# Kernel optimization log

Measured on AMD Instinct MI355X. Metric: run time of the kernel, lower is better.

Reference implementation:

```python
import jax, jax.numpy as jnp
import numpy as np

B, T, IN, OUT, R = 8, 2048, 4096, 4096, 64


def setup_inputs() -> dict:
    key = jax.random.key(0)
    ks = jax.random.split(key, 6)
    x = jax.random.normal(ks[0], (B, T, IN), dtype=jnp.float32)
    weight_main = jax.random.normal(ks[1], (OUT, IN), dtype=jnp.float32) * (1.0 / np.sqrt(IN))
    U = jax.random.normal(ks[2], (OUT, R), dtype=jnp.float32) * 0.02
    S = jax.random.uniform(ks[3], (R,), dtype=jnp.float32)
    V = jax.random.normal(ks[4], (R, IN), dtype=jnp.float32) * 0.02
    bias = jax.random.normal(ks[5], (OUT,), dtype=jnp.float32) * 0.01
    return {"x": x, "weight_main": weight_main, "U": U, "S": S, "V": V, "bias": bias}


def reference(x, weight_main, U, S, V, bias):
    # residual_weight = einsum('ij,j,jk->ik', U, S, V): full [out, in] materialization
    residual_weight = jnp.einsum('ij,j,jk->ik', U, S, V)
    weight = weight_main + residual_weight
    # F.linear: x @ weight.T + bias
    return jnp.einsum('bti,oi->bto', x, weight) + bias
```

## Files before the change

kernel.cpp:

```cpp
#include <hip/hip_runtime.h>
#include <hip/hip_bf16.h>
#include <stdint.h>

#define DI __device__ __forceinline__

typedef __attribute__((ext_vector_type(4))) float f32x4;
typedef __attribute__((ext_vector_type(8))) short bf16x8;
typedef __attribute__((ext_vector_type(4))) short s16x4;

typedef unsigned short ushort_t;

constexpr int M_ = 16384;
constexpr int N_ = 4096;
constexpr int K_ = 4096;
constexpr int R_ = 64;

constexpr int BM = 256, BN = 256, BK = 64;
constexpr int NSEG = 3;
constexpr int NT_SEG = K_ / BK;
constexpr int TOT_T = NSEG * NT_SEG;

DI ushort_t f32_to_bf16_rne(float f) {
    unsigned u = __builtin_bit_cast(unsigned, f);
    u += 0x7FFFu + ((u >> 16) & 1u);
    return (ushort_t)(u >> 16);
}
DI float bf16_to_f32(ushort_t h) {
    return __builtin_bit_cast(float, (unsigned)h << 16);
}

DI void async_cp16(const void* g, void* l) {
    __builtin_amdgcn_global_load_lds(
        (const __attribute__((address_space(1))) unsigned*)g,
        (__attribute__((address_space(3))) unsigned*)l, 16, 0, 0);
}

#define BAR() do { asm volatile("" ::: "memory"); \
                   __builtin_amdgcn_s_barrier(); \
                   asm volatile("" ::: "memory"); } while (0)
#define MID() do { BAR(); \
                   asm volatile("s_waitcnt lgkmcnt(0)" ::: "memory"); \
                   __builtin_amdgcn_sched_barrier(0); \
                   __builtin_amdgcn_s_setprio(1); } while (0)
#define ENDP() do { __builtin_amdgcn_s_setprio(0); BAR(); } while (0)

__global__ __launch_bounds__(256) void k_fold_us(const float* __restrict__ U,
                                                 const float* __restrict__ S,
                                                 float* __restrict__ US) {
    int i = blockIdx.x * 256 + threadIdx.x;
    if (i < N_ * R_) US[i] = U[i] * S[i & (R_ - 1)];
}

__global__ __launch_bounds__(256) void k_fuse_w(const float* __restrict__ WM,
                                                const float* __restrict__ US,
                                                const float* __restrict__ V,
                                                ushort_t* __restrict__ hiW,
                                                ushort_t* __restrict__ loW) {
    __shared__ __align__(16) float sUS[64][68];
    __shared__ __align__(16) float sV[64][128];
    int t = threadIdx.x;
    int n0 = (blockIdx.x >> 5) * 64;
    int k0 = (blockIdx.x & 31) * 128;
#pragma unroll
    for (int j = 0; j < 4; ++j) {
        int f = j * 1024 + t * 4;
        int r = f >> 6, c = f & 63;
        *(f32x4*)&sUS[r][c] = *(const f32x4*)&US[(size_t)(n0 + r) * R_ + c];
    }
#pragma unroll
    for (int j = 0; j < 8; ++j) {
        int f = j * 1024 + t * 4;
        int r = f >> 7, c = f & 127;
        *(f32x4*)&sV[r][c] = *(const f32x4*)&V[(size_t)r * K_ + k0 + c];
    }
    __syncthreads();
    int tn = t >> 5;
    int tk = t & 31;
    float acc[8][4] = {};
    for (int r = 0; r < R_; ++r) {
        f32x4 vv = *(const f32x4*)&sV[r][tk * 4];
#pragma unroll
        for (int a = 0; a < 8; ++a) {
            float u = sUS[tn * 8 + a][r];
#pragma unroll
            for (int c = 0; c < 4; ++c) acc[a][c] += u * vv[c];
        }
    }
#pragma unroll
    for (int a = 0; a < 8; ++a) {
        int n = n0 + tn * 8 + a;
        int k = k0 + tk * 4;
        f32x4 wmv = *(const f32x4*)&WM[(size_t)n * K_ + k];
        s16x4 h4, l4;
#pragma unroll
        for (int c = 0; c < 4; ++c) {
            float w = wmv[c] + acc[a][c];
            ushort_t h = f32_to_bf16_rne(w);
            h4[c] = (short)h;
            l4[c] = (short)f32_to_bf16_rne(w - bf16_to_f32(h));
        }
        *(s16x4*)&hiW[(size_t)n * K_ + k] = h4;
        *(s16x4*)&loW[(size_t)n * K_ + k] = l4;
    }
}

__global__ __launch_bounds__(256) void k_split_x(const float* __restrict__ X,
                                                 ushort_t* __restrict__ hiA,
                                                 ushort_t* __restrict__ loA) {
    size_t i = ((size_t)blockIdx.x * 256 + threadIdx.x) * 8;
    f32x4 a = *(const f32x4*)&X[i];
    f32x4 b = *(const f32x4*)&X[i + 4];
    bf16x8 h, l;
#pragma unroll
    for (int j = 0; j < 4; ++j) {
        ushort_t ha = f32_to_bf16_rne(a[j]);
        ushort_t hb = f32_to_bf16_rne(b[j]);
        h[j]     = (short)ha;
        h[4 + j] = (short)hb;
        l[j]     = (short)f32_to_bf16_rne(a[j] - bf16_to_f32(ha));
        l[4 + j] = (short)f32_to_bf16_rne(b[j] - bf16_to_f32(hb));
    }
    *(bf16x8*)&hiA[i] = h;
    *(bf16x8*)&loA[i] = l;
}

__global__ __launch_bounds__(512, 2) void k_gemm_8ph(const ushort_t* __restrict__ hiA,
                                                     const ushort_t* __restrict__ loA,
                                                     const ushort_t* __restrict__ hiW,
                                                     const ushort_t* __restrict__ loW,
                                                     const float* __restrict__ bias,
                                                     float* __restrict__ out) {
    __shared__ __align__(16) ushort_t lA[2][BM * BK];
    __shared__ __align__(16) ushort_t lB[2][BN * BK];

    int bid = blockIdx.x;
    int wg  = (bid & 7) * (gridDim.x >> 3) + (bid >> 3);
    int m0  = (wg >> 4) * BM;
    int n0  = (wg & 15) * BN;

    int tid  = threadIdx.x;
    int lane = tid & 63;
    int w    = tid >> 6;
    int wr   = w >> 2;
    int wc   = w & 3;
    int fr   = lane & 15;
    int fq   = lane >> 4;

    f32x4 acc[8][4] = {};

    auto stageA = [&](int tau, int h) {
        int seg = tau >> 6;
        const ushort_t* As = (seg == 1) ? loA : hiA;
        int k0 = (tau & (NT_SEG - 1)) * BK;
        ushort_t* dst = &lA[tau & 1][h * (128 * 64)];
#pragma unroll
        for (int j = 0; j < 2; ++j) {
            int ci  = j * 512 + tid;
            int row = ci >> 3, pc = ci & 7;
            int lc  = pc ^ (row & 7);
            async_cp16(&As[(size_t)(m0 + h * 128 + row) * K_ + k0 + lc * 8], &dst[ci * 8]);
        }
    };
    auto stageB = [&](int tau, int h) {
        int seg = tau >> 6;
        const ushort_t* Bs = (seg == 2) ? loW : hiW;
        int k0 = (tau & (NT_SEG - 1)) * BK;
        ushort_t* dst = &lB[tau & 1][h * (128 * 64)];
#pragma unroll
        for (int j = 0; j < 2; ++j) {
            int ci  = j * 512 + tid;
            int row = ci >> 3, pc = ci & 7;
            int lc  = pc ^ (row & 7);
            async_cp16(&Bs[(size_t)(n0 + h * 128 + row) * K_ + k0 + lc * 8], &dst[ci * 8]);
        }
    };
    auto rdA = [&](const ushort_t* la, int i, int ks) -> bf16x8 {
        int row = wr * 128 + i * 16 + fr;
        return *(const bf16x8*)&la[row * 64 + (((ks * 4 + fq) ^ (row & 7)) << 3)];
    };
    auto rdB = [&](const ushort_t* lb, int j, int ks) -> bf16x8 {
        int row = wc * 64 + j * 16 + fr;
        return *(const bf16x8*)&lb[row * 64 + (((ks * 4 + fq) ^ (row & 7)) << 3)];
    };

    bf16x8 aF[4][2];
    bf16x8 bE[2][2];
    bf16x8 bO[2][2];

    stageB(0, 0); stageB(0, 1); stageA(0, 0); stageA(0, 1);
    stageB(1, 0); stageB(1, 1);
    asm volatile("s_waitcnt vmcnt(4)" ::: "memory");
    BAR();

    const ushort_t* la0 = lA[0]; const ushort_t* lb0 = lB[0];
    const ushort_t* la1 = lA[1]; const ushort_t* lb1 = lB[1];

    constexpr int NIT = TOT_T / 2;
    for (int it = 0; it < NIT; ++it) {
        int to = 2 * it + 1;
        int ne = (2 * it + 2) % TOT_T;
        int no = (2 * it + 3) % TOT_T;

#pragma unroll
        for (int i = 0; i < 4; ++i) { aF[i][0] = rdA(la0, i, 0); aF[i][1] = rdA(la0, i, 1); }
#pragma unroll
        for (int j = 0; j < 2; ++j) { bE[j][0] = rdB(lb0, j, 0); bE[j][1] = rdB(lb0, j, 1); }
        stageA(to, 0);
        asm volatile("s_waitcnt lgkmcnt(8)" ::: "memory");
        MID();
#pragma unroll
        for (int i = 0; i < 4; ++i)
#pragma unroll
            for (int j = 0; j < 2; ++j)
#pragma unroll
                for (int ks = 0; ks < 2; ++ks)
                    acc[i][j] = __builtin_amdgcn_mfma_f32_16x16x32_bf16(aF[i][ks], bE[j][ks], acc[i][j], 0, 0, 0);
        ENDP();

#pragma unroll
        for (int j = 0; j < 2; ++j) { bO[j][0] = rdB(lb0, 2 + j, 0); bO[j][1] = rdB(lb0, 2 + j, 1); }
        stageA(to, 1);
        MID();
#pragma unroll
        for (int i = 0; i < 4; ++i)
#pragma unroll
            for (int j = 0; j < 2; ++j)
#pragma unroll
                for (int ks = 0; ks < 2; ++ks)
                    acc[i][2 + j] = __builtin_amdgcn_mfma_f32_16x16x32_bf16(aF[i][ks], bO[j][ks], acc[i][2 + j], 0, 0, 0);
        ENDP();

#pragma unroll
        for (int i = 0; i < 4; ++i) { aF[i][0] = rdA(la0, 4 + i, 0); aF[i][1] = rdA(la0, 4 + i, 1); }
        stageB(ne, 0);
        MID();
#pragma unroll
        for (int i = 0; i < 4; ++i)
#pragma unroll
            for (int j = 0; j < 2; ++j)
#pragma unroll
                for (int ks = 0; ks < 2; ++ks)
                    acc[4 + i][2 + j] = __builtin_amdgcn_mfma_f32_16x16x32_bf16(aF[i][ks], bO[j][ks], acc[4 + i][2 + j], 0, 0, 0);
        ENDP();

        stageB(ne, 1);
        asm volatile("s_waitcnt vmcnt(4)" ::: "memory");
        MID();
#pragma unroll
        for (int i = 0; i < 4; ++i)
#pragma unroll
            for (int j = 0; j < 2; ++j)
#pragma unroll
                for (int ks = 0; ks < 2; ++ks)
                    acc[4 + i][j] = __builtin_amdgcn_mfma_f32_16x16x32_bf16(aF[i][ks], bE[j][ks], acc[4 + i][j], 0, 0, 0);
        ENDP();

#pragma unroll
        for (int i = 0; i < 4; ++i) { aF[i][0] = rdA(la1, i, 0); aF[i][1] = rdA(la1, i, 1); }
#pragma unroll
        for (int j = 0; j < 2; ++j) { bE[j][0] = rdB(lb1, j, 0); bE[j][1] = rdB(lb1, j, 1); }
        stageA(ne, 0);
        asm volatile("s_waitcnt lgkmcnt(8)" ::: "memory");
        MID();
#pragma unroll
        for (int i = 0; i < 4; ++i)
#pragma unroll
            for (int j = 0; j < 2; ++j)
#pragma unroll
                for (int ks = 0; ks < 2; ++ks)
                    acc[i][j] = __builtin_amdgcn_mfma_f32_16x16x32_bf16(aF[i][ks], bE[j][ks], acc[i][j], 0, 0, 0);
        ENDP();

#pragma unroll
        for (int j = 0; j < 2; ++j) { bO[j][0] = rdB(lb1, 2 + j, 0); bO[j][1] = rdB(lb1, 2 + j, 1); }
        stageA(ne, 1);
        MID();
#pragma unroll
        for (int i = 0; i < 4; ++i)
#pragma unroll
            for (int j = 0; j < 2; ++j)
#pragma unroll
                for (int ks = 0; ks < 2; ++ks)
                    acc[i][2 + j] = __builtin_amdgcn_mfma_f32_16x16x32_bf16(aF[i][ks], bO[j][ks], acc[i][2 + j], 0, 0, 0);
        ENDP();

#pragma unroll
        for (int i = 0; i < 4; ++i) { aF[i][0] = rdA(la1, 4 + i, 0); aF[i][1] = rdA(la1, 4 + i, 1); }
        stageB(no, 0);
        MID();
#pragma unroll
        for (int i = 0; i < 4; ++i)
#pragma unroll
            for (int j = 0; j < 2; ++j)
#pragma unroll
                for (int ks = 0; ks < 2; ++ks)
                    acc[4 + i][2 + j] = __builtin_amdgcn_mfma_f32_16x16x32_bf16(aF[i][ks], bO[j][ks], acc[4 + i][2 + j], 0, 0, 0);
        ENDP();

        stageB(no, 1);
        asm volatile("s_waitcnt vmcnt(4)" ::: "memory");
        MID();
#pragma unroll
        for (int i = 0; i < 4; ++i)
#pragma unroll
            for (int j = 0; j < 2; ++j)
#pragma unroll
                for (int ks = 0; ks < 2; ++ks)
                    acc[4 + i][j] = __builtin_amdgcn_mfma_f32_16x16x32_bf16(aF[i][ks], bE[j][ks], acc[4 + i][j], 0, 0, 0);
        ENDP();
    }

    asm volatile("s_waitcnt vmcnt(0)" ::: "memory");

    float bcol[4];
#pragma unroll
    for (int j = 0; j < 4; ++j) bcol[j] = bias[n0 + wc * 64 + j * 16 + fr];
#pragma unroll
    for (int i = 0; i < 8; ++i) {
        int gm = m0 + wr * 128 + i * 16 + fq * 4;
#pragma unroll
        for (int j = 0; j < 4; ++j) {
            int gn = n0 + wc * 64 + j * 16 + fr;
#pragma unroll
            for (int r2 = 0; r2 < 4; ++r2)
                out[(size_t)(gm + r2) * N_ + gn] = acc[i][j][r2] + bcol[j];
        }
    }
}

__global__ __launch_bounds__(256, 2) void k_gemm_small(const float* __restrict__ X,
                                                       const ushort_t* __restrict__ hiW,
                                                       const ushort_t* __restrict__ loW,
                                                       const float* __restrict__ bias,
                                                       float* __restrict__ out) {
    __shared__ __align__(16) ushort_t lA[128 * 64];
    __shared__ __align__(16) ushort_t lB[128 * 64];
    int bid = blockIdx.x;
    int cpx = gridDim.x >> 3;
    int wg  = (bid & 7) * cpx + (bid >> 3);
    constexpr int NBN = N_ / 128;
    int m0 = (wg / NBN) * 128;
    int n0 = (wg % NBN) * 128;
    int tid  = threadIdx.x;
    int lane = tid & 63;
    int w    = tid >> 6;
    int wr   = w >> 1, wc = w & 1;
    int fr   = lane & 15;
    int fq   = lane >> 4;
    f32x4 acc[4][4] = {};
    for (int seg = 0; seg < 3; ++seg) {
        const ushort_t* Bs = (seg == 2) ? loW : hiW;
        bool wantLo = (seg == 1);
        for (int kt = 0; kt < K_ / 64; ++kt) {
            int k0 = kt * 64;
#pragma unroll
            for (int j = 0; j < 4; ++j) {
                int f = j * 2048 + tid * 8;
                int row = f >> 6, col = f & 63;
                async_cp16(&Bs[(size_t)(n0 + row) * K_ + k0 + col], &lB[f]);
            }
#pragma unroll
            for (int j = 0; j < 4; ++j) {
                int f = j * 2048 + tid * 8;
                int row = f >> 6, c = f & 63;
                const float* xp = &X[(size_t)(m0 + row) * K_ + k0 + c];
                f32x4 x0 = *(const f32x4*)xp;
                f32x4 x1 = *(const f32x4*)(xp + 4);
                bf16x8 o;
#pragma unroll
                for (int e = 0; e < 4; ++e) {
                    ushort_t h0 = f32_to_bf16_rne(x0[e]);
                    ushort_t h1 = f32_to_bf16_rne(x1[e]);
                    o[e]     = (short)(wantLo ? f32_to_bf16_rne(x0[e] - bf16_to_f32(h0)) : h0);
                    o[4 + e] = (short)(wantLo ? f32_to_bf16_rne(x1[e] - bf16_to_f32(h1)) : h1);
                }
                *(bf16x8*)&lA[f] = o;
            }
            __syncthreads();
#pragma unroll
            for (int ks = 0; ks < 2; ++ks) {
                bf16x8 af[4], bfv[4];
#pragma unroll
                for (int i = 0; i < 4; ++i) {
                    af[i]  = *(const bf16x8*)&lA[(wr * 64 + i * 16 + fr) * 64 + ks * 32 + fq * 8];
                    bfv[i] = *(const bf16x8*)&lB[(wc * 64 + i * 16 + fr) * 64 + ks * 32 + fq * 8];
                }
#pragma unroll
                for (int i = 0; i < 4; ++i)
#pragma unroll
                    for (int j = 0; j < 4; ++j)
                        acc[i][j] = __builtin_amdgcn_mfma_f32_16x16x32_bf16(af[i], bfv[j], acc[i][j], 0, 0, 0);
            }
            __syncthreads();
        }
    }
    float bcol[4];
#pragma unroll
    for (int j = 0; j < 4; ++j) bcol[j] = bias[n0 + wc * 64 + j * 16 + fr];
#pragma unroll
    for (int i = 0; i < 4; ++i) {
        int gm = m0 + wr * 64 + i * 16 + fq * 4;
#pragma unroll
        for (int j = 0; j < 4; ++j) {
            int gn = n0 + wc * 64 + j * 16 + fr;
#pragma unroll
            for (int r2 = 0; r2 < 4; ++r2)
                out[(size_t)(gm + r2) * N_ + gn] = acc[i][j][r2] + bcol[j];
        }
    }
}

__global__ __launch_bounds__(256) void k_naive(const float* __restrict__ X,
                                               const float* __restrict__ WM,
                                               const float* __restrict__ U,
                                               const float* __restrict__ S,
                                               const float* __restrict__ V,
                                               const float* __restrict__ bias,
                                               float* __restrict__ out) {
    __shared__ __align__(16) float sX[64][68];
    __shared__ __align__(16) float sW[64][68];
    __shared__ __align__(16) float sV[64][68];
    int t = threadIdx.x;
    int m0 = (blockIdx.x >> 6) * 64;
    int n0 = (blockIdx.x & 63) * 64;
    int tm = t >> 4, tn = t & 15;
    float acc[4][4] = {}, pacc[4][4] = {};
    for (int kc = 0; kc < K_ / 64; ++kc) {
        __syncthreads();
#pragma unroll
        for (int j = 0; j < 4; ++j) {
            int f = j * 1024 + t * 4;
            int r = f >> 6, c = f & 63;
            *(f32x4*)&sX[r][c] = *(const f32x4*)&X[(size_t)(m0 + r) * K_ + kc * 64 + c];
            *(f32x4*)&sW[r][c] = *(const f32x4*)&WM[(size_t)(n0 + r) * K_ + kc * 64 + c];
            *(f32x4*)&sV[r][c] = *(const f32x4*)&V[(size_t)r * K_ + kc * 64 + c];
        }
        __syncthreads();
        for (int k4 = 0; k4 < 16; ++k4) {
            f32x4 xa[4], wb[4], vb[4];
#pragma unroll
            for (int a = 0; a < 4; ++a) xa[a] = *(const f32x4*)&sX[tm * 4 + a][k4 * 4];
#pragma unroll
            for (int b = 0; b < 4; ++b) {
                wb[b] = *(const f32x4*)&sW[tn * 4 + b][k4 * 4];
                vb[b] = *(const f32x4*)&sV[tn * 4 + b][k4 * 4];
            }
#pragma unroll
            for (int a = 0; a < 4; ++a)
#pragma unroll
                for (int b = 0; b < 4; ++b)
#pragma unroll
                    for (int e = 0; e < 4; ++e) {
                        acc[a][b]  += xa[a][e] * wb[b][e];
                        pacc[a][b] += xa[a][e] * vb[b][e];
                    }
        }
    }
    __syncthreads();
#pragma unroll
    for (int j = 0; j < 4; ++j) {
        int f = j * 1024 + t * 4;
        int nl = f >> 6, r = f & 63;
        f32x4 uu = *(const f32x4*)&U[(size_t)(n0 + nl) * R_ + r];
        f32x4 ss = *(const f32x4*)&S[r];
        f32x4 us = uu * ss;
        *(f32x4*)&sV[nl][r] = us;
    }
#pragma unroll
    for (int a = 0; a < 4; ++a)
#pragma unroll
        for (int b = 0; b < 4; ++b) sW[tm * 4 + a][tn * 4 + b] = pacc[a][b];
    __syncthreads();
#pragma unroll
    for (int a = 0; a < 4; ++a)
#pragma unroll
        for (int b = 0; b < 4; ++b) {
            float s2 = acc[a][b];
            for (int r = 0; r < R_; ++r) s2 += sW[tm * 4 + a][r] * sV[tn * 4 + b][r];
            out[(size_t)(m0 + tm * 4 + a) * N_ + n0 + tn * 4 + b] = s2 + bias[n0 + tn * 4 + b];
        }
}

extern "C" void kernel_launch(void* const* d_in, const int* in_sizes, int n_in,
                              void* d_out, int out_size, void* d_ws, size_t ws_size,
                              hipStream_t stream) {
    const float* x    = (const float*)d_in[0];
    const float* wm   = (const float*)d_in[1];
    const float* U    = (const float*)d_in[2];
    const float* S    = (const float*)d_in[3];
    const float* V    = (const float*)d_in[4];
    const float* bias = (const float*)d_in[5];
    float* out = (float*)d_out;

    const size_t szA  = (size_t)M_ * K_ * 2;
    const size_t szW  = (size_t)N_ * K_ * 2;
    const size_t szUS = (size_t)N_ * R_ * 4;

    if (ws_size >= 2 * szA + 2 * szW + szUS) {
        ushort_t* hiA = (ushort_t*)d_ws;
        ushort_t* loA = (ushort_t*)((char*)d_ws + szA);
        ushort_t* hiW = (ushort_t*)((char*)d_ws + 2 * szA);
        ushort_t* loW = (ushort_t*)((char*)d_ws + 2 * szA + szW);
        float*    US  = (float*)((char*)d_ws + 2 * szA + 2 * szW);
        k_fold_us<<<dim3((N_ * R_ + 255) / 256), dim3(256), 0, stream>>>(U, S, US);
        k_fuse_w<<<dim3((N_ / 64) * (K_ / 128)), dim3(256), 0, stream>>>(wm, US, V, hiW, loW);
        k_split_x<<<dim3(M_ * K_ / 2048), dim3(256), 0, stream>>>(x, hiA, loA);
        k_gemm_8ph<<<dim3((M_ / BM) * (N_ / BN)), dim3(512), 0, stream>>>(
            hiA, loA, hiW, loW, bias, out);
    } else if (ws_size >= 2 * szW + szUS) {
        ushort_t* hiW = (ushort_t*)d_ws;
        ushort_t* loW = (ushort_t*)((char*)d_ws + szW);
        float*    US  = (float*)((char*)d_ws + 2 * szW);
        k_fold_us<<<dim3((N_ * R_ + 255) / 256), dim3(256), 0, stream>>>(U, S, US);
        k_fuse_w<<<dim3((N_ / 64) * (K_ / 128)), dim3(256), 0, stream>>>(wm, US, V, hiW, loW);
        k_gemm_small<<<dim3((M_ / 128) * (N_ / 128)), dim3(256), 0, stream>>>(
            x, hiW, loW, bias, out);
    } else {
        k_naive<<<dim3((M_ / 64) * (N_ / 64)), dim3(256), 0, stream>>>(x, wm, U, S, V, bias, out);
    }
}
```

Baseline: 1.873 ms.

## Prefetch LDS fragments one phase ahead in GEMM loop and fold U*S into fuse kernel

```diff
diff --git a/kernel.cpp b/kernel.cpp
--- a/kernel.cpp
+++ b/kernel.cpp
@@ -44,15 +44,9 @@
                    __builtin_amdgcn_s_setprio(1); } while (0)
 #define ENDP() do { __builtin_amdgcn_s_setprio(0); BAR(); } while (0)
 
-__global__ __launch_bounds__(256) void k_fold_us(const float* __restrict__ U,
-                                                 const float* __restrict__ S,
-                                                 float* __restrict__ US) {
-    int i = blockIdx.x * 256 + threadIdx.x;
-    if (i < N_ * R_) US[i] = U[i] * S[i & (R_ - 1)];
-}
-
 __global__ __launch_bounds__(256) void k_fuse_w(const float* __restrict__ WM,
-                                                const float* __restrict__ US,
+                                                const float* __restrict__ U,
+                                                const float* __restrict__ S,
                                                 const float* __restrict__ V,
                                                 ushort_t* __restrict__ hiW,
                                                 ushort_t* __restrict__ loW) {
@@ -65,7 +59,9 @@
     for (int j = 0; j < 4; ++j) {
         int f = j * 1024 + t * 4;
         int r = f >> 6, c = f & 63;
-        *(f32x4*)&sUS[r][c] = *(const f32x4*)&US[(size_t)(n0 + r) * R_ + c];
+        f32x4 uu = *(const f32x4*)&U[(size_t)(n0 + r) * R_ + c];
+        f32x4 ss = *(const f32x4*)&S[c];
+        *(f32x4*)&sUS[r][c] = uu * ss;
     }
 #pragma unroll
     for (int j = 0; j < 8; ++j) {
@@ -183,17 +179,30 @@
         return *(const bf16x8*)&lb[row * 64 + (((ks * 4 + fq) ^ (row & 7)) << 3)];
     };
 
-    bf16x8 aF[4][2];
-    bf16x8 bE[2][2];
-    bf16x8 bO[2][2];
+    bf16x8 aX[4], aY[4], bX[4], bY[4];
+
+#define RD_A(dst, la, ib, ks) do { \
+    dst[0] = rdA(la, (ib) + 0, ks); dst[1] = rdA(la, (ib) + 1, ks); \
+    dst[2] = rdA(la, (ib) + 2, ks); dst[3] = rdA(la, (ib) + 3, ks); } while (0)
+#define RD_B(dst, lb, ks) do { \
+    dst[0] = rdB(lb, 0, ks); dst[1] = rdB(lb, 1, ks); \
+    dst[2] = rdB(lb, 2, ks); dst[3] = rdB(lb, 3, ks); } while (0)
+#define MFMA16(IB, A_, B_) do { \
+    _Pragma("unroll") \
+    for (int i_ = 0; i_ < 4; ++i_) \
+        _Pragma("unroll") \
+        for (int j_ = 0; j_ < 4; ++j_) \
+            acc[(IB) + i_][j_] = __builtin_amdgcn_mfma_f32_16x16x32_bf16( \
+                A_[i_], B_[j_], acc[(IB) + i_][j_], 0, 0, 0); } while (0)
+
+    const ushort_t* la0 = lA[0]; const ushort_t* lb0 = lB[0];
+    const ushort_t* la1 = lA[1]; const ushort_t* lb1 = lB[1];
 
     stageB(0, 0); stageB(0, 1); stageA(0, 0); stageA(0, 1);
     stageB(1, 0); stageB(1, 1);
     asm volatile("s_waitcnt vmcnt(4)" ::: "memory");
     BAR();
-
-    const ushort_t* la0 = lA[0]; const ushort_t* lb0 = lB[0];
-    const ushort_t* la1 = lA[1]; const ushort_t* lb1 = lB[1];
+    RD_A(aX, la0, 0, 0); RD_B(bX, lb0, 0);
 
     constexpr int NIT = TOT_T / 2;
     for (int it = 0; it < NIT; ++it) {
@@ -201,116 +210,55 @@
         int ne = (2 * it + 2) % TOT_T;
         int no = (2 * it + 3) % TOT_T;
 
-#pragma unroll
-        for (int i = 0; i < 4; ++i) { aF[i][0] = rdA(la0, i, 0); aF[i][1] = rdA(la0, i, 1); }
-#pragma unroll
-        for (int j = 0; j < 2; ++j) { bE[j][0] = rdB(lb0, j, 0); bE[j][1] = rdB(lb0, j, 1); }
         stageA(to, 0);
-        asm volatile("s_waitcnt lgkmcnt(8)" ::: "memory");
-        MID();
-#pragma unroll
-        for (int i = 0; i < 4; ++i)
-#pragma unroll
-            for (int j = 0; j < 2; ++j)
-#pragma unroll
-                for (int ks = 0; ks < 2; ++ks)
-                    acc[i][j] = __builtin_amdgcn_mfma_f32_16x16x32_bf16(aF[i][ks], bE[j][ks], acc[i][j], 0, 0, 0);
-        ENDP();
-
-#pragma unroll
-        for (int j = 0; j < 2; ++j) { bO[j][0] = rdB(lb0, 2 + j, 0); bO[j][1] = rdB(lb0, 2 + j, 1); }
+        MID();
+        RD_A(aY, la0, 4, 0);
+        MFMA16(0, aX, bX);
+        ENDP();
         stageA(to, 1);
         MID();
-#pragma unroll
-        for (int i = 0; i < 4; ++i)
-#pragma unroll
-            for (int j = 0; j < 2; ++j)
-#pragma unroll
-                for (int ks = 0; ks < 2; ++ks)
-                    acc[i][2 + j] = __builtin_amdgcn_mfma_f32_16x16x32_bf16(aF[i][ks], bO[j][ks], acc[i][2 + j], 0, 0, 0);
-        ENDP();
-
-#pragma unroll
-        for (int i = 0; i < 4; ++i) { aF[i][0] = rdA(la0, 4 + i, 0); aF[i][1] = rdA(la0, 4 + i, 1); }
+        RD_A(aX, la0, 0, 1); RD_B(bY, lb0, 1);
+        MFMA16(4, aY, bX);
+        ENDP();
         stageB(ne, 0);
         MID();
-#pragma unroll
-        for (int i = 0; i < 4; ++i)
-#pragma unroll
-            for (int j = 0; j < 2; ++j)
-#pragma unroll
-                for (int ks = 0; ks < 2; ++ks)
-                    acc[4 + i][2 + j] = __builtin_amdgcn_mfma_f32_16x16x32_bf16(aF[i][ks], bO[j][ks], acc[4 + i][2 + j], 0, 0, 0);
-        ENDP();
-
+        RD_A(aY, la0, 4, 1);
+        MFMA16(0, aX, bY);
+        ENDP();
         stageB(ne, 1);
         asm volatile("s_waitcnt vmcnt(4)" ::: "memory");
         MID();
-#pragma unroll
-        for (int i = 0; i < 4; ++i)
-#pragma unroll
-            for (int j = 0; j < 2; ++j)
-#pragma unroll
-                for (int ks = 0; ks < 2; ++ks)
-                    acc[4 + i][j] = __builtin_amdgcn_mfma_f32_16x16x32_bf16(aF[i][ks], bE[j][ks], acc[4 + i][j], 0, 0, 0);
-        ENDP();
-
-#pragma unroll
-        for (int i = 0; i < 4; ++i) { aF[i][0] = rdA(la1, i, 0); aF[i][1] = rdA(la1, i, 1); }
-#pragma unroll
-        for (int j = 0; j < 2; ++j) { bE[j][0] = rdB(lb1, j, 0); bE[j][1] = rdB(lb1, j, 1); }
+        RD_A(aX, la1, 0, 0); RD_B(bX, lb1, 0);
+        MFMA16(4, aY, bY);
+        ENDP();
         stageA(ne, 0);
-        asm volatile("s_waitcnt lgkmcnt(8)" ::: "memory");
-        MID();
-#pragma unroll
-        for (int i = 0; i < 4; ++i)
-#pragma unroll
-            for (int j = 0; j < 2; ++j)
-#pragma unroll
-                for (int ks = 0; ks < 2; ++ks)
-                    acc[i][j] = __builtin_amdgcn_mfma_f32_16x16x32_bf16(aF[i][ks], bE[j][ks], acc[i][j], 0, 0, 0);
-        ENDP();
-
-#pragma unroll
-        for (int j = 0; j < 2; ++j) { bO[j][0] = rdB(lb1, 2 + j, 0); bO[j][1] = rdB(lb1, 2 + j, 1); }
+        MID();
+        RD_A(aY, la1, 4, 0);
+        MFMA16(0, aX, bX);
+        ENDP();
         stageA(ne, 1);
         MID();
-#pragma unroll
-        for (int i = 0; i < 4; ++i)
-#pragma unroll
-            for (int j = 0; j < 2; ++j)
-#pragma unroll
-                for (int ks = 0; ks < 2; ++ks)
-                    acc[i][2 + j] = __builtin_amdgcn_mfma_f32_16x16x32_bf16(aF[i][ks], bO[j][ks], acc[i][2 + j], 0, 0, 0);
-        ENDP();
-
-#pragma unroll
-        for (int i = 0; i < 4; ++i) { aF[i][0] = rdA(la1, 4 + i, 0); aF[i][1] = rdA(la1, 4 + i, 1); }
+        RD_A(aX, la1, 0, 1); RD_B(bY, lb1, 1);
+        MFMA16(4, aY, bX);
+        ENDP();
         stageB(no, 0);
         MID();
-#pragma unroll
-        for (int i = 0; i < 4; ++i)
-#pragma unroll
-            for (int j = 0; j < 2; ++j)
-#pragma unroll
-                for (int ks = 0; ks < 2; ++ks)
-                    acc[4 + i][2 + j] = __builtin_amdgcn_mfma_f32_16x16x32_bf16(aF[i][ks], bO[j][ks], acc[4 + i][2 + j], 0, 0, 0);
-        ENDP();
-
+        RD_A(aY, la1, 4, 1);
+        MFMA16(0, aX, bY);
+        ENDP();
         stageB(no, 1);
         asm volatile("s_waitcnt vmcnt(4)" ::: "memory");
         MID();
-#pragma unroll
-        for (int i = 0; i < 4; ++i)
-#pragma unroll
-            for (int j = 0; j < 2; ++j)
-#pragma unroll
-                for (int ks = 0; ks < 2; ++ks)
-                    acc[4 + i][j] = __builtin_amdgcn_mfma_f32_16x16x32_bf16(aF[i][ks], bE[j][ks], acc[4 + i][j], 0, 0, 0);
+        RD_A(aX, la0, 0, 0); RD_B(bX, lb0, 0);
+        MFMA16(4, aY, bY);
         ENDP();
     }
 
     asm volatile("s_waitcnt vmcnt(0)" ::: "memory");
+
+#undef RD_A
+#undef RD_B
+#undef MFMA16
 
     float bcol[4];
 #pragma unroll
@@ -492,27 +440,22 @@
     const float* bias = (const float*)d_in[5];
     float* out = (float*)d_out;
 
-    const size_t szA  = (size_t)M_ * K_ * 2;
-    const size_t szW  = (size_t)N_ * K_ * 2;
-    const size_t szUS = (size_t)N_ * R_ * 4;
-
-    if (ws_size >= 2 * szA + 2 * szW + szUS) {
+    const size_t szA = (size_t)M_ * K_ * 2;
+    const size_t szW = (size_t)N_ * K_ * 2;
+
+    if (ws_size >= 2 * szA + 2 * szW) {
         ushort_t* hiA = (ushort_t*)d_ws;
         ushort_t* loA = (ushort_t*)((char*)d_ws + szA);
         ushort_t* hiW = (ushort_t*)((char*)d_ws + 2 * szA);
         ushort_t* loW = (ushort_t*)((char*)d_ws + 2 * szA + szW);
-        float*    US  = (float*)((char*)d_ws + 2 * szA + 2 * szW);
-        k_fold_us<<<dim3((N_ * R_ + 255) / 256), dim3(256), 0, stream>>>(U, S, US);
-        k_fuse_w<<<dim3((N_ / 64) * (K_ / 128)), dim3(256), 0, stream>>>(wm, US, V, hiW, loW);
+        k_fuse_w<<<dim3((N_ / 64) * (K_ / 128)), dim3(256), 0, stream>>>(wm, U, S, V, hiW, loW);
         k_split_x<<<dim3(M_ * K_ / 2048), dim3(256), 0, stream>>>(x, hiA, loA);
         k_gemm_8ph<<<dim3((M_ / BM) * (N_ / BN)), dim3(512), 0, stream>>>(
             hiA, loA, hiW, loW, bias, out);
-    } else if (ws_size >= 2 * szW + szUS) {
+    } else if (ws_size >= 2 * szW) {
         ushort_t* hiW = (ushort_t*)d_ws;
         ushort_t* loW = (ushort_t*)((char*)d_ws + szW);
-        float*    US  = (float*)((char*)d_ws + 2 * szW);
-        k_fold_us<<<dim3((N_ * R_ + 255) / 256), dim3(256), 0, stream>>>(U, S, US);
-        k_fuse_w<<<dim3((N_ / 64) * (K_ / 128)), dim3(256), 0, stream>>>(wm, US, V, hiW, loW);
+        k_fuse_w<<<dim3((N_ / 64) * (K_ / 128)), dim3(256), 0, stream>>>(wm, U, S, V, hiW, loW);
         k_gemm_small<<<dim3((M_ / 128) * (N_ / 128)), dim3(256), 0, stream>>>(
             x, hiW, loW, bias, out);
     } else {
```

Result: no change. 1.872 ms (-0.0%).
